# Performance work log

Measured on AMD Instinct MI355X. Metric: run time of the kernel, lower is better.

## Reference

```python
import jax, jax.numpy as jnp
import numpy as np
import math

D_MODEL = 576
N_HEADS = 9
HEAD_DIM = D_MODEL // N_HEADS  # 64
KV_DIM = HEAD_DIM              # compression ratio 1
EPS = 1e-6


def setup_inputs() -> dict:
    key = jax.random.key(0)
    k1, k2, k3, k4 = jax.random.split(key, 4)
    B, S = 16, 2048
    x = jax.random.normal(k1, (B, S, D_MODEL), dtype=jnp.float32)
    scale = 0.02
    Wq = jax.random.normal(k2, (D_MODEL, D_MODEL), dtype=jnp.float32) * scale
    Wkv = jax.random.normal(k3, (N_HEADS * 2 * KV_DIM, D_MODEL), dtype=jnp.float32) * scale
    Wo = jax.random.normal(k4, (D_MODEL, D_MODEL), dtype=jnp.float32) * scale
    return {"x": x, "Wq": Wq, "Wkv": Wkv, "Wo": Wo}


def _rope(q):
    # q: [B, S, H, D]; rotate pairs with theta_i = 10000^{-2i/D}
    B, S, H, D = q.shape
    theta = 1.0 / (10000.0 ** (jnp.arange(0, D, 2, dtype=jnp.float32) / D))  # [D/2]
    freqs = jnp.arange(S, dtype=jnp.float32)[:, None] * theta[None, :]       # [S, D/2]
    cos = jnp.cos(freqs)[None, :, None, :]
    sin = jnp.sin(freqs)[None, :, None, :]
    qr = q.reshape(B, S, H, D // 2, 2)
    a, b = qr[..., 0], qr[..., 1]  # real / imag parts
    ra = a * cos - b * sin
    rb = a * sin + b * cos
    return jnp.stack([ra, rb], axis=-1).reshape(B, S, H, D)


def reference(x, Wq, Wkv, Wo):
    B, S, _ = x.shape
    identity = x
    # RMSNorm (weight is freshly-initialized ones in the source)
    norm = jnp.sqrt(jnp.mean(x * x, axis=-1, keepdims=True) + EPS)
    xn = x / norm
    q = (xn @ Wq.T).reshape(B, S, N_HEADS, HEAD_DIM)
    kv = (xn @ Wkv.T).reshape(B, S, N_HEADS, 2 * KV_DIM)
    k, v = kv[..., :KV_DIM], kv[..., KV_DIM:]
    q = _rope(q)
    # faithful to source: q is NOT moved to [B,H,S,D]; matmul contracts head_dim
    # per position -> head-vs-head scores [B, S, H, H]
    scores = jnp.einsum('bshd,bsgd->bshg', q, k) / math.sqrt(HEAD_DIM)
    w = jax.nn.softmax(scores.astype(jnp.float32), axis=-1).astype(x.dtype)
    attn = jnp.einsum('bshg,bsgd->bshd', w, v)  # [B, S, H, D]
    # source: transpose(1,2).contiguous().view(B, S, d_model)
    attn = jnp.transpose(attn, (0, 2, 1, 3)).reshape(B, S, D_MODEL)
    out = attn @ Wo.T
    return out + identity
```

## Files before the change

### kernel.cpp

```cpp
#include <hip/hip_runtime.h>

typedef __bf16 bf16;
typedef __attribute__((ext_vector_type(4))) float  f32x4;
typedef __attribute__((ext_vector_type(8))) short  s16x8;
typedef __attribute__((ext_vector_type(8))) __bf16 bf16x8;
typedef __attribute__((ext_vector_type(4))) __bf16 bf16x4;

#define MROWS 32768
#define KD    576
#define N1P   1792
#define N2P   640

__device__ __forceinline__ void gload_lds16(const void* g, void* l) {
  __builtin_amdgcn_global_load_lds((const __attribute__((address_space(1))) void*)g,
                                   (__attribute__((address_space(3))) void*)l, 16, 0, 0);
}

__global__ __launch_bounds__(256) void rmsnorm_k(const float* __restrict__ x,
                                                 bf16* __restrict__ xn) {
  const int lane = threadIdx.x & 63;
  const int row  = blockIdx.x * 4 + (threadIdx.x >> 6);
  const float4* xr = (const float4*)(x + (size_t)row * KD);
  float4 v0 = xr[lane];
  float4 v1 = xr[lane + 64];
  float4 v2 = {0.f, 0.f, 0.f, 0.f};
  if (lane < 16) v2 = xr[lane + 128];
  float ss = v0.x*v0.x + v0.y*v0.y + v0.z*v0.z + v0.w*v0.w
           + v1.x*v1.x + v1.y*v1.y + v1.z*v1.z + v1.w*v1.w
           + v2.x*v2.x + v2.y*v2.y + v2.z*v2.z + v2.w*v2.w;
#pragma unroll
  for (int off = 32; off > 0; off >>= 1) ss += __shfl_xor(ss, off, 64);
  const float inv = 1.0f / sqrtf(ss * (1.0f / 576.0f) + 1e-6f);
  bf16* orow = xn + (size_t)row * KD;
  bf16x4 o0 = {(bf16)(v0.x*inv), (bf16)(v0.y*inv), (bf16)(v0.z*inv), (bf16)(v0.w*inv)};
  *(bf16x4*)(orow + lane * 4) = o0;
  bf16x4 o1 = {(bf16)(v1.x*inv), (bf16)(v1.y*inv), (bf16)(v1.z*inv), (bf16)(v1.w*inv)};
  *(bf16x4*)(orow + (lane + 64) * 4) = o1;
  if (lane < 16) {
    bf16x4 o2 = {(bf16)(v2.x*inv), (bf16)(v2.y*inv), (bf16)(v2.z*inv), (bf16)(v2.w*inv)};
    *(bf16x4*)(orow + (lane + 128) * 4) = o2;
  }
}

__global__ void rope_k(float* __restrict__ ctab, float* __restrict__ stab) {
  const int s = blockIdx.x * blockDim.x + threadIdx.x;
  if (s >= 2048) return;
#pragma unroll 1
  for (int i = 0; i < 32; ++i) {
    const float theta = powf(10000.0f, -(float)i * (1.0f / 32.0f));
    const float f = (float)s * theta;
    float sv, cv;
    sincosf(f, &sv, &cv);
    ctab[s * 32 + i] = cv;
    stab[s * 32 + i] = sv;
  }
}

__global__ __launch_bounds__(256) void wconv_k(const float* __restrict__ Wq,
                                               const float* __restrict__ Wkv,
                                               const float* __restrict__ Wo,
                                               bf16* __restrict__ wcat,
                                               bf16* __restrict__ wo) {
  const int idx = blockIdx.x * 256 + threadIdx.x;
  {
    const int row = idx / 576;
    float v = 0.f;
    if (row < 576)       v = Wq[idx];
    else if (row < 1728) v = Wkv[idx - 331776];
    wcat[idx] = (bf16)v;
  }
  if (idx < 640 * 576) {
    float v = (idx < 331776) ? Wo[idx] : 0.f;
    wo[idx] = (bf16)v;
  }
}

template <int EPI>
__global__ __launch_bounds__(256) void gemm_k(const bf16* __restrict__ A,
                                              const bf16* __restrict__ Bw,
                                              void* __restrict__ Cp,
                                              const float* __restrict__ ident,
                                              int ntiles, int ldc) {
  __shared__ bf16 As[128 * 64];
  __shared__ bf16 Bs[128 * 64];
  const int tid  = threadIdx.x;
  const int lane = tid & 63;
  const int nwg = gridDim.x;
  const int cpx = nwg >> 3;
  const int swz = (blockIdx.x & 7) * cpx + (blockIdx.x >> 3);
  const int mt = swz / ntiles;
  const int nt = swz - mt * ntiles;
  const int wv = tid >> 6;
  const int wr = (wv >> 1) << 6;
  const int wc = (wv & 1) << 6;

  const size_t abase = (size_t)mt * 128 * KD;
  const size_t bbase = (size_t)nt * 128 * KD;

  f32x4 zero = {0.f, 0.f, 0.f, 0.f};
  f32x4 acc[4][4];
#pragma unroll
  for (int i = 0; i < 4; ++i)
#pragma unroll
    for (int j = 0; j < 4; ++j) acc[i][j] = zero;

  for (int kt = 0; kt < 9; ++kt) {
    const int k0 = kt * 64;
    __syncthreads();
#pragma unroll
    for (int r = 0; r < 4; ++r) {
      const int c   = r * 256 + tid;
      const int row = c >> 3;
      const int ks  = (c & 7) ^ (row & 7);
      gload_lds16(A + abase + (size_t)row * KD + k0 + ks * 8, As + c * 8);
    }
#pragma unroll
    for (int r = 0; r < 4; ++r) {
      const int c   = r * 256 + tid;
      const int row = c >> 3;
      const int ks  = (c & 7) ^ (row & 7);
      gload_lds16(Bw + bbase + (size_t)row * KD + k0 + ks * 8, Bs + c * 8);
    }
    __syncthreads();
#pragma unroll
    for (int kk = 0; kk < 2; ++kk) {
      s16x8 af[4], bq[4];
#pragma unroll
      for (int i = 0; i < 4; ++i) {
        const int arow = wr + i * 16 + (lane & 15);
        const int aps  = ((kk << 2) + (lane >> 4)) ^ (arow & 7);
        af[i] = *(const s16x8*)(As + arow * 64 + aps * 8);
      }
#pragma unroll
      for (int j = 0; j < 4; ++j) {
        const int brow = wc + j * 16 + (lane & 15);
        const int bps  = ((kk << 2) + (lane >> 4)) ^ (brow & 7);
        bq[j] = *(const s16x8*)(Bs + brow * 64 + bps * 8);
      }
#pragma unroll
      for (int i = 0; i < 4; ++i)
#pragma unroll
        for (int j = 0; j < 4; ++j)
          acc[i][j] = __builtin_amdgcn_mfma_f32_16x16x32_bf16(af[i], bq[j], acc[i][j], 0, 0, 0);
    }
  }
  const int rbase = mt * 128 + wr + ((lane >> 4) << 2);
  const int cbase = nt * 128 + wc + (lane & 15);
  if (EPI == 0) {
    bf16* C = (bf16*)Cp;
#pragma unroll
    for (int i = 0; i < 4; ++i)
#pragma unroll
      for (int j = 0; j < 4; ++j)
#pragma unroll
        for (int r = 0; r < 4; ++r)
          C[(size_t)(rbase + i * 16 + r) * ldc + (cbase + j * 16)] = (bf16)acc[i][j][r];
  } else {
    float* C = (float*)Cp;
#pragma unroll
    for (int i = 0; i < 4; ++i)
#pragma unroll
      for (int j = 0; j < 4; ++j) {
        const int col = cbase + j * 16;
        if (col < 576) {
#pragma unroll
          for (int r = 0; r < 4; ++r) {
            const size_t off = (size_t)(rbase + i * 16 + r) * 576 + col;
            C[off] = acc[i][j][r] + ident[off];
          }
        }
      }
  }
}

__global__ __launch_bounds__(256) void attn_k(const bf16* __restrict__ qkv,
                                              const float* __restrict__ ctab,
                                              const float* __restrict__ stab,
                                              bf16* __restrict__ attn) {
  const int tid = blockIdx.x * 256 + threadIdx.x;
  const int bs  = tid / 9;
  const int h   = tid - bs * 9;
  const int s   = bs & 2047;
  const bf16* qrow = qkv + (size_t)bs * N1P;

  float q[64];
#pragma unroll
  for (int c = 0; c < 8; ++c) {
    bf16x8 v = *(const bf16x8*)(qrow + h * 64 + c * 8);
#pragma unroll
    for (int e = 0; e < 8; ++e) q[c * 8 + e] = (float)v[e];
  }
  const float* cr = ctab + s * 32;
  const float* sr = stab + s * 32;
#pragma unroll
  for (int i = 0; i < 32; ++i) {
    const float cv = cr[i], sv = sr[i];
    const float a = q[2 * i], b = q[2 * i + 1];
    q[2 * i]     = a * cv - b * sv;
    q[2 * i + 1] = a * sv + b * cv;
  }
  const bf16* kvr = qrow + 576;
  float sc[9];
#pragma unroll
  for (int g = 0; g < 9; ++g) {
    const bf16* kg = kvr + g * 128;
    float d0 = 0.f, d1 = 0.f, d2 = 0.f, d3 = 0.f;
#pragma unroll
    for (int c = 0; c < 8; ++c) {
      bf16x8 v = *(const bf16x8*)(kg + c * 8);
      d0 += q[c*8+0] * (float)v[0];
      d1 += q[c*8+1] * (float)v[1];
      d2 += q[c*8+2] * (float)v[2];
      d3 += q[c*8+3] * (float)v[3];
      d0 += q[c*8+4] * (float)v[4];
      d1 += q[c*8+5] * (float)v[5];
      d2 += q[c*8+6] * (float)v[6];
      d3 += q[c*8+7] * (float)v[7];
    }
    sc[g] = (d0 + d1 + d2 + d3) * 0.125f;
  }
  float mx = sc[0];
#pragma unroll
  for (int g = 1; g < 9; ++g) mx = fmaxf(mx, sc[g]);
  float sum = 0.f;
#pragma unroll
  for (int g = 0; g < 9; ++g) { sc[g] = expf(sc[g] - mx); sum += sc[g]; }
  const float inv = 1.0f / sum;

  float oacc[64];
#pragma unroll
  for (int e = 0; e < 64; ++e) oacc[e] = 0.f;
#pragma unroll
  for (int g = 0; g < 9; ++g) {
    const float w = sc[g] * inv;
    const bf16* vg = kvr + g * 128 + 64;
#pragma unroll
    for (int c = 0; c < 8; ++c) {
      bf16x8 v = *(const bf16x8*)(vg + c * 8);
#pragma unroll
      for (int e = 0; e < 8; ++e) oacc[c * 8 + e] += w * (float)v[e];
    }
  }
  const int b = bs >> 11;
  bf16* orow = attn + ((size_t)((b * 9 + h) * 2048 + s)) * 64;
#pragma unroll
  for (int c = 0; c < 8; ++c) {
    bf16x8 o;
#pragma unroll
    for (int e = 0; e < 8; ++e) o[e] = (bf16)oacc[c * 8 + e];
    *(bf16x8*)(orow + c * 8) = o;
  }
}

extern "C" void kernel_launch(void* const* d_in, const int* in_sizes, int n_in,
                              void* d_out, int out_size, void* d_ws, size_t ws_size,
                              hipStream_t stream) {
  const float* x   = (const float*)d_in[0];
  const float* Wq  = (const float*)d_in[1];
  const float* Wkv = (const float*)d_in[2];
  const float* Wo  = (const float*)d_in[3];

  char* ws = (char*)d_ws;
  const size_t o_xn   = 0;
  const size_t o_wcat = o_xn   + 37748736;
  const size_t o_wo   = o_wcat + 2064384;
  const size_t o_ct   = o_wo   + 737280;
  const size_t o_st   = o_ct   + 262144;
  const size_t o_qkv  = o_st   + 262144;
  const size_t need   = o_qkv  + 117440512;
  if (ws_size < need) return;

  bf16*  xn   = (bf16*)(ws + o_xn);
  bf16*  attn = (bf16*)(ws + o_xn);
  bf16*  wcat = (bf16*)(ws + o_wcat);
  bf16*  wo   = (bf16*)(ws + o_wo);
  float* ctab = (float*)(ws + o_ct);
  float* stab = (float*)(ws + o_st);
  bf16*  qkv  = (bf16*)(ws + o_qkv);

  rmsnorm_k<<<8192, 256, 0, stream>>>(x, xn);
  rope_k<<<32, 64, 0, stream>>>(ctab, stab);
  wconv_k<<<4032, 256, 0, stream>>>(Wq, Wkv, Wo, wcat, wo);
  gemm_k<0><<<3584, 256, 0, stream>>>(xn, wcat, (void*)qkv, nullptr, 14, N1P);
  attn_k<<<1152, 256, 0, stream>>>(qkv, ctab, stab, attn);
  gemm_k<1><<<1280, 256, 0, stream>>>(attn, wo, d_out, x, 5, 576);
}
```

Before: 355.5 us.

## Replace QKV GEMM with 256x256 double-buffered 8-wave pipelined kernel

The QKV projection GEMM now uses a new 512-thread kernel with 256x256 tiles. It double-buffers 128KB of dynamic LDS, interleaves the next tile's global-to-LDS loads between MFMA phases, raises wave priority around the MFMAs, and stages the epilogue through LDS so stores are coalesced. The attention kernel now accumulates the V-weighted sum per 8-element chunk instead of holding a 64-float accumulator, which cuts register pressure. The rope table uses exp2f instead of powf. The aim is higher MFMA utilisation and better data reuse in the dominant GEMM, at the cost of heavy LDS use that limits occupancy, plus manual barrier and waitcnt scheduling that is fragile.

```diff
diff --git a/kernel.cpp b/kernel.cpp
--- a/kernel.cpp
+++ b/kernel.cpp
@@ -6,10 +6,11 @@
 typedef __attribute__((ext_vector_type(8))) __bf16 bf16x8;
 typedef __attribute__((ext_vector_type(4))) __bf16 bf16x4;
 
-#define MROWS 32768
 #define KD    576
 #define N1P   1792
-#define N2P   640
+
+#define BAR()    __builtin_amdgcn_s_barrier()
+#define SCHED0() __builtin_amdgcn_sched_barrier(0)
 
 __device__ __forceinline__ void gload_lds16(const void* g, void* l) {
   __builtin_amdgcn_global_load_lds((const __attribute__((address_space(1))) void*)g,
@@ -42,12 +43,13 @@
   }
 }
 
-__global__ void rope_k(float* __restrict__ ctab, float* __restrict__ stab) {
+__global__ void ropetab_k(float* __restrict__ ctab, float* __restrict__ stab) {
   const int s = blockIdx.x * blockDim.x + threadIdx.x;
   if (s >= 2048) return;
+  const float l2r = 0.4152410118609203f;
 #pragma unroll 1
   for (int i = 0; i < 32; ++i) {
-    const float theta = powf(10000.0f, -(float)i * (1.0f / 32.0f));
+    const float theta = exp2f(-(float)i * l2r);
     const float f = (float)s * theta;
     float sv, cv;
     sincosf(f, &sv, &cv);
@@ -75,12 +77,141 @@
   }
 }
 
-template <int EPI>
-__global__ __launch_bounds__(256) void gemm_k(const bf16* __restrict__ A,
-                                              const bf16* __restrict__ Bw,
-                                              void* __restrict__ Cp,
-                                              const float* __restrict__ ident,
-                                              int ntiles, int ldc) {
+__global__ __launch_bounds__(512, 2) void gemm8p_k(const bf16* __restrict__ A,
+                                                   const bf16* __restrict__ Bw,
+                                                   bf16* __restrict__ C,
+                                                   int ntiles) {
+  extern __shared__ char smem[];
+  const int tid  = threadIdx.x;
+  const int lane = tid & 63;
+  const int wv   = tid >> 6;
+  const int nwg = gridDim.x;
+  const int cpx = nwg >> 3;
+  const int swz = (blockIdx.x & 7) * cpx + (blockIdx.x >> 3);
+  const int mt = swz / ntiles;
+  const int nt = swz - mt * ntiles;
+  const int wMl = (wv >> 2) << 7;
+  const int wNl = (wv & 3) << 6;
+
+  const bf16* Ab = A  + (size_t)mt * 256 * KD;
+  const bf16* Bb = Bw + (size_t)nt * 256 * KD;
+
+  int off[4];
+#pragma unroll
+  for (int u = 0; u < 2; ++u)
+#pragma unroll
+    for (int q = 0; q < 2; ++q) {
+      const int c = u * 1024 + q * 512 + tid;
+      const int row = c >> 3, slot = c & 7;
+      const int ks = slot ^ (row & 7);
+      off[u * 2 + q] = row * KD + ks * 8;
+    }
+
+  auto stage_unit = [&](int uu, int k0n, int bb) {
+    const int u = uu & 1;
+#pragma unroll
+    for (int q = 0; q < 2; ++q) {
+      const int c = u * 1024 + q * 512 + tid;
+      if (uu < 2) gload_lds16(Ab + off[u * 2 + q] + k0n, smem + bb * 65536 + c * 16);
+      else        gload_lds16(Bb + off[u * 2 + q] + k0n, smem + bb * 65536 + 32768 + c * 16);
+    }
+  };
+
+  f32x4 acc[8][4];
+#pragma unroll
+  for (int i = 0; i < 8; ++i)
+#pragma unroll
+    for (int j = 0; j < 4; ++j) { acc[i][j][0]=0.f; acc[i][j][1]=0.f; acc[i][j][2]=0.f; acc[i][j][3]=0.f; }
+
+#pragma unroll
+  for (int uu = 0; uu < 4; ++uu) stage_unit(uu, 0, 0);
+
+#pragma unroll 1
+  for (int t = 0; t < 9; ++t) {
+    const int cur = t & 1, nxt = cur ^ 1;
+    const int k0n = (t + 1) * 64;
+    if (t < 8) {
+      stage_unit(0, k0n, nxt);
+      stage_unit(1, k0n, nxt);
+      asm volatile("s_waitcnt vmcnt(4)" ::: "memory");
+    } else {
+      asm volatile("s_waitcnt vmcnt(0)" ::: "memory");
+    }
+    BAR();
+    const bf16* As = (const bf16*)(smem + cur * 65536);
+    const bf16* Bs = (const bf16*)(smem + cur * 65536 + 32768);
+    s16x8 bfrag[4][2];
+#pragma unroll
+    for (int p = 0; p < 4; ++p) {
+      s16x8 afrag[2][2];
+#pragma unroll
+      for (int i2 = 0; i2 < 2; ++i2)
+#pragma unroll
+        for (int kk = 0; kk < 2; ++kk) {
+          const int arow = wMl + (p * 2 + i2) * 16 + (lane & 15);
+          const int aps  = ((kk << 2) + (lane >> 4)) ^ (arow & 7);
+          afrag[i2][kk] = *(const s16x8*)(As + arow * 64 + aps * 8);
+        }
+      if (p == 0) {
+#pragma unroll
+        for (int j = 0; j < 4; ++j)
+#pragma unroll
+          for (int kk = 0; kk < 2; ++kk) {
+            const int brow = wNl + j * 16 + (lane & 15);
+            const int bps  = ((kk << 2) + (lane >> 4)) ^ (brow & 7);
+            bfrag[j][kk] = *(const s16x8*)(Bs + brow * 64 + bps * 8);
+          }
+      }
+      if (t < 8 && p < 2) stage_unit(2 + p, k0n, nxt);
+      BAR();
+      asm volatile("s_waitcnt lgkmcnt(0)" ::: "memory");
+      SCHED0();
+      __builtin_amdgcn_s_setprio(1);
+#pragma unroll
+      for (int i2 = 0; i2 < 2; ++i2)
+#pragma unroll
+        for (int j = 0; j < 4; ++j)
+#pragma unroll
+          for (int kk = 0; kk < 2; ++kk)
+            acc[p * 2 + i2][j] = __builtin_amdgcn_mfma_f32_16x16x32_bf16(
+                afrag[i2][kk], bfrag[j][kk], acc[p * 2 + i2][j], 0, 0, 0);
+      __builtin_amdgcn_s_setprio(0);
+      SCHED0();
+      BAR();
+    }
+  }
+
+  bf16* ep = (bf16*)(smem + wv * 9216);
+  const size_t crow0 = (size_t)(mt * 256 + wMl);
+  const int    ccol0 = nt * 256 + wNl;
+#pragma unroll 1
+  for (int half = 0; half < 2; ++half) {
+    asm volatile("s_waitcnt lgkmcnt(0)" ::: "memory"); SCHED0();
+#pragma unroll
+    for (int i = 0; i < 4; ++i)
+#pragma unroll
+      for (int j = 0; j < 4; ++j)
+#pragma unroll
+        for (int r = 0; r < 4; ++r) {
+          const int row = i * 16 + ((lane >> 4) << 2) + r;
+          ep[row * 72 + j * 16 + (lane & 15)] = (bf16)acc[half * 4 + i][j][r];
+        }
+    asm volatile("s_waitcnt lgkmcnt(0)" ::: "memory"); SCHED0();
+#pragma unroll
+    for (int it = 0; it < 8; ++it) {
+      const int c = it * 64 + lane;
+      const int row = c >> 3, c8 = c & 7;
+      s16x8 v = *(const s16x8*)(ep + row * 72 + c8 * 8);
+      *(s16x8*)(C + (crow0 + half * 64 + row) * (size_t)N1P + ccol0 + c8 * 8) = v;
+    }
+  }
+}
+
+__global__ __launch_bounds__(256) void gemm_o_k(const bf16* __restrict__ A,
+                                                const bf16* __restrict__ Bw,
+                                                float* __restrict__ C,
+                                                const float* __restrict__ ident,
+                                                int ntiles) {
   __shared__ bf16 As[128 * 64];
   __shared__ bf16 Bs[128 * 64];
   const int tid  = threadIdx.x;
@@ -146,37 +277,25 @@
   }
   const int rbase = mt * 128 + wr + ((lane >> 4) << 2);
   const int cbase = nt * 128 + wc + (lane & 15);
-  if (EPI == 0) {
-    bf16* C = (bf16*)Cp;
-#pragma unroll
-    for (int i = 0; i < 4; ++i)
-#pragma unroll
-      for (int j = 0; j < 4; ++j)
-#pragma unroll
-        for (int r = 0; r < 4; ++r)
-          C[(size_t)(rbase + i * 16 + r) * ldc + (cbase + j * 16)] = (bf16)acc[i][j][r];
-  } else {
-    float* C = (float*)Cp;
-#pragma unroll
-    for (int i = 0; i < 4; ++i)
-#pragma unroll
-      for (int j = 0; j < 4; ++j) {
-        const int col = cbase + j * 16;
-        if (col < 576) {
-#pragma unroll
-          for (int r = 0; r < 4; ++r) {
-            const size_t off = (size_t)(rbase + i * 16 + r) * 576 + col;
-            C[off] = acc[i][j][r] + ident[off];
-          }
+#pragma unroll
+  for (int i = 0; i < 4; ++i)
+#pragma unroll
+    for (int j = 0; j < 4; ++j) {
+      const int col = cbase + j * 16;
+      if (col < 576) {
+#pragma unroll
+        for (int r = 0; r < 4; ++r) {
+          const size_t o = (size_t)(rbase + i * 16 + r) * 576 + col;
+          C[o] = acc[i][j][r] + ident[o];
         }
       }
-  }
-}
-
-__global__ __launch_bounds__(256) void attn_k(const bf16* __restrict__ qkv,
-                                              const float* __restrict__ ctab,
-                                              const float* __restrict__ stab,
-                                              bf16* __restrict__ attn) {
+    }
+}
+
+__global__ __launch_bounds__(256) void attn2_k(const bf16* __restrict__ qkv,
+                                               const float* __restrict__ ctab,
+                                               const float* __restrict__ stab,
+                                               bf16* __restrict__ attn) {
   const int tid = blockIdx.x * 256 + threadIdx.x;
   const int bs  = tid / 9;
   const int h   = tid - bs * 9;
@@ -226,29 +345,26 @@
 #pragma unroll
   for (int g = 0; g < 9; ++g) { sc[g] = expf(sc[g] - mx); sum += sc[g]; }
   const float inv = 1.0f / sum;
-
-  float oacc[64];
-#pragma unroll
-  for (int e = 0; e < 64; ++e) oacc[e] = 0.f;
-#pragma unroll
-  for (int g = 0; g < 9; ++g) {
-    const float w = sc[g] * inv;
-    const bf16* vg = kvr + g * 128 + 64;
-#pragma unroll
-    for (int c = 0; c < 8; ++c) {
-      bf16x8 v = *(const bf16x8*)(vg + c * 8);
-#pragma unroll
-      for (int e = 0; e < 8; ++e) oacc[c * 8 + e] += w * (float)v[e];
-    }
-  }
+#pragma unroll
+  for (int g = 0; g < 9; ++g) sc[g] *= inv;
+
   const int b = bs >> 11;
   bf16* orow = attn + ((size_t)((b * 9 + h) * 2048 + s)) * 64;
 #pragma unroll
   for (int c = 0; c < 8; ++c) {
-    bf16x8 o;
-#pragma unroll
-    for (int e = 0; e < 8; ++e) o[e] = (bf16)oacc[c * 8 + e];
-    *(bf16x8*)(orow + c * 8) = o;
+    float o[8];
+#pragma unroll
+    for (int e = 0; e < 8; ++e) o[e] = 0.f;
+#pragma unroll
+    for (int g = 0; g < 9; ++g) {
+      bf16x8 v = *(const bf16x8*)(kvr + g * 128 + 64 + c * 8);
+#pragma unroll
+      for (int e = 0; e < 8; ++e) o[e] += sc[g] * (float)v[e];
+    }
+    bf16x8 ov;
+#pragma unroll
+    for (int e = 0; e < 8; ++e) ov[e] = (bf16)o[e];
+    *(bf16x8*)(orow + c * 8) = ov;
   }
 }
 
@@ -278,10 +394,13 @@
   float* stab = (float*)(ws + o_st);
   bf16*  qkv  = (bf16*)(ws + o_qkv);
 
+  hipFuncSetAttribute((const void*)gemm8p_k,
+                      hipFuncAttributeMaxDynamicSharedMemorySize, 131072);
+
   rmsnorm_k<<<8192, 256, 0, stream>>>(x, xn);
-  rope_k<<<32, 64, 0, stream>>>(ctab, stab);
+  ropetab_k<<<32, 64, 0, stream>>>(ctab, stab);
   wconv_k<<<4032, 256, 0, stream>>>(Wq, Wkv, Wo, wcat, wo);
-  gemm_k<0><<<3584, 256, 0, stream>>>(xn, wcat, (void*)qkv, nullptr, 14, N1P);
-  attn_k<<<1152, 256, 0, stream>>>(qkv, ctab, stab, attn);
-  gemm_k<1><<<1280, 256, 0, stream>>>(attn, wo, d_out, x, 5, 576);
-}
+  gemm8p_k<<<896, 512, 131072, stream>>>(xn, wcat, qkv, 7);
+  attn2_k<<<1152, 256, 0, stream>>>(qkv, ctab, stab, attn);
+  gemm_o_k<<<1280, 256, 0, stream>>>(attn, wo, (float*)d_out, x, 5);
+}
```

Result: slower. 450.1 us (+26.6%).
